# Optimization experiments

Measured on AMD Instinct MI355X. Metric: run time of the kernel, lower is better.

Reference implementation:

```python
import jax, jax.numpy as jnp
import numpy as np

DIS_NORM = 6.0 * 512 / 1000.0  # 6 * D(z=0) * Nmesh / Boxsize with D(0)=1


def setup_inputs() -> dict:
    key = jax.random.key(0)
    x = jax.random.normal(key, (2, 4, 128, 128, 128), dtype=jnp.float32)
    return {"x": x}


def _lag2eul(x):
    N, C = x.shape[0], x.shape[1]
    D, H, W = x.shape[2], x.shape[3], x.shape[4]
    P = D * H * W
    Cout = C - 3 if C > 3 else 1

    # rm_dis_mean=True: mean displacement, detached
    dis_mean = jax.lax.stop_gradient(jnp.mean(x[:, :3], axis=(2, 3, 4), keepdims=True))

    pos = (x[:, :3] - dis_mean) * DIS_NORM  # (N,3,D,H,W)
    gd = jnp.arange(D, dtype=x.dtype) + 0.5
    gh = jnp.arange(H, dtype=x.dtype) + 0.5
    gw = jnp.arange(W, dtype=x.dtype) + 0.5
    grid = jnp.stack(jnp.meshgrid(gd, gh, gw, indexing='ij'))  # (3,D,H,W)
    pos = (pos + grid[None]).reshape(N, 3, P)

    if C > 3:
        val = x[:, 3:].reshape(N, Cout, P)
    else:
        val = jnp.ones((N, Cout, P), dtype=x.dtype)

    intpos = jnp.floor(pos).astype(jnp.int32)
    # 8 trilinear neighbors: bit b of n -> offset along dim b
    neighbors = (jnp.arange(8, dtype=jnp.int32)[None, :] >> jnp.arange(3, dtype=jnp.int32)[:, None]) & 1  # (3,8)
    tgt = intpos[:, :, :, None] + neighbors[None, :, None, :]  # (N,3,P,8)

    kernel = jnp.prod(1.0 - jnp.abs(pos[:, :, :, None] - tgt.astype(x.dtype)), axis=1)  # (N,P,8)
    src = val[:, :, :, None] * kernel[:, None, :, :]  # (N,Cout,P,8)

    # periodic=False: mask out-of-bounds deposits
    bounds = jnp.array([D, H, W], dtype=jnp.int32)[None, :, None, None]
    mask = jnp.all((tgt >= 0) & (tgt < bounds), axis=1)  # (N,P,8)
    ind = (tgt[:, 0] * H + tgt[:, 1]) * W + tgt[:, 2]  # (N,P,8)
    ind = jnp.clip(ind, 0, P - 1)
    src = jnp.where(mask[:, None, :, :], src, jnp.zeros((), dtype=x.dtype))

    def scatter_one(ind_n, src_n):
        mesh = jnp.zeros((Cout, P), dtype=src_n.dtype)
        return mesh.at[:, ind_n.reshape(-1)].add(src_n.reshape(Cout, -1))

    mesh = jax.vmap(scatter_one)(ind, src)  # (N,Cout,P)
    return mesh.reshape(N, Cout, D, H, W)


def reference(x):
    return _lag2eul(x)
```

## Files before the change

kernel.cpp:

```cpp
#include <hip/hip_runtime.h>
#include <hip/hip_fp16.h>

#define NBATCH 2
#define NDIM   128
#define NP     (128 * 128 * 128)
#define DIS_NORM 3.072f

#define TS   16
#define LO   5
#define HI   6
#define WIN  (TS + LO + HI)
#define WIN2 (WIN * WIN)
#define WINF (WIN * WIN * WIN)
#define TPB  8
#define NTILE (TPB * TPB * TPB)
#define NTHR 512

#define FXSCALE 16777216.0f
#define FXINV   (1.0f / 16777216.0f)

#define QCAP 176

#define SLABH 19704

#define SUMS_OFF 0
#define SLABS_OFF 1024
#define WS_FLOATS ((size_t)SLABS_OFF + (size_t)NBATCH * NTILE * SLABH / 2)
#define WS_NEEDED_BYTES (WS_FLOATS * sizeof(float))

__device__ __constant__ int BASE27[27] = {
    0,216,792,976,1552,3088,3568,3752,4232,
    4384,4960,6496,6976,8512,12608,13888,14368,15648,
    16048,16232,16712,16864,17344,18624,19024,19176,19576};

__global__ __launch_bounds__(256) void prep_kernel(const float* __restrict__ x,
                                                   float* __restrict__ ws,
                                                   float* __restrict__ out) {
    const int plane = blockIdx.y;
    if (plane < 6) {
        const int n = plane / 3, c = plane % 3;
        const float4* xp = (const float4*)(x + ((size_t)n * 4 + c) * NP);
        float s = 0.0f;
        for (int i = blockIdx.x * 256 + threadIdx.x; i < NP / 4; i += 128 * 256) {
            float4 v = xp[i];
            s += (v.x + v.y) + (v.z + v.w);
        }
        #pragma unroll
        for (int off = 32; off > 0; off >>= 1) s += __shfl_down(s, off, 64);
        __shared__ float wsum[4];
        if ((threadIdx.x & 63) == 0) wsum[threadIdx.x >> 6] = s;
        __syncthreads();
        if (threadIdx.x == 0)
            ws[SUMS_OFF + plane * 128 + blockIdx.x] =
                (wsum[0] + wsum[1]) + (wsum[2] + wsum[3]);
    } else {
        float4* o4 = (float4*)out;
        const float4 z = make_float4(0.f, 0.f, 0.f, 0.f);
        for (int i = blockIdx.x * 256 + threadIdx.x; i < NBATCH * NP / 4; i += 128 * 256)
            o4[i] = z;
    }
}

__device__ __forceinline__ void load_means128(const float* __restrict__ ws, int n,
                                              float& m0, float& m1, float& m2) {
    float s0 = 0.f, s1 = 0.f, s2 = 0.f;
    const float* p0 = ws + SUMS_OFF + (n * 3 + 0) * 128;
    const float* p1 = ws + SUMS_OFF + (n * 3 + 1) * 128;
    const float* p2 = ws + SUMS_OFF + (n * 3 + 2) * 128;
    #pragma unroll 4
    for (int b = 0; b < 128; ++b) { s0 += p0[b]; s1 += p1[b]; s2 += p2[b]; }
    const float inv_np = 1.0f / (float)NP;
    m0 = s0 * inv_np; m1 = s1 * inv_np; m2 = s2 * inv_np;
}

__device__ __forceinline__ void deposit_pair(unsigned long long* __restrict__ winU,
                                             int b, float va, float vb) {
    const int fa = __float2int_rn(va * FXSCALE);
    const int fb = __float2int_rn(vb * FXSCALE);
    const bool odd = (b & 1);
    const long long packed = (((long long)fb) << 32) + (long long)fa;
    const long long hiOnly = ((long long)fa) << 32;
    atomicAdd(&winU[b >> 1], (unsigned long long)(odd ? hiOnly : packed));
    if (odd) atomicAdd(&winU[(b >> 1) + 1], (unsigned long long)(long long)fb);
}

__device__ __forceinline__ void slow_deposit(unsigned long long* __restrict__ winU,
                                             float* __restrict__ sp,
                                             float pd, float ph, float pw, float v,
                                             int od, int oh, int ow) {
    const float fd = floorf(pd), fh = floorf(ph), fw = floorf(pw);
    const int id = (int)fd, ih = (int)fh, iw = (int)fw;
    const float rd = pd - fd, rh = ph - fh, rw = pw - fw;
    const int wd = id - od, wh = ih - oh, ww = iw - ow;
    const float wd2[2] = {1.0f - rd, rd};
    const float wh2[2] = {1.0f - rh, rh};
    const float ww2[2] = {1.0f - rw, rw};
    #pragma unroll
    for (int dd = 0; dd < 2; ++dd) {
        const int td = id + dd, wdc = wd + dd;
        const bool dW = (unsigned)wdc < WIN, dM = (unsigned)td < NDIM;
        if (!dM && !dW) continue;
        #pragma unroll
        for (int hh = 0; hh < 2; ++hh) {
            const int th = ih + hh, whc = wh + hh;
            const bool hW = (unsigned)whc < WIN, hM = (unsigned)th < NDIM;
            const float vdh = v * wd2[dd] * wh2[hh];
            #pragma unroll
            for (int wi = 0; wi < 2; ++wi) {
                const int tw = iw + wi, wwc = ww + wi;
                const bool wW = (unsigned)wwc < WIN, wM = (unsigned)tw < NDIM;
                const float dep = vdh * ww2[wi];
                if (dW && hW && wW) {
                    const int cb = (wdc * WIN + whc) * WIN + wwc;
                    const int fx = __float2int_rn(dep * FXSCALE);
                    const long long cv = (cb & 1)
                        ? (((long long)fx) << 32) : (long long)fx;
                    atomicAdd(&winU[cb >> 1], (unsigned long long)cv);
                } else if (dM && hM && wM) {
                    atomicAdd(sp + ((size_t)td * NDIM + th) * NDIM + tw, dep);
                }
            }
        }
    }
}

__global__ __launch_bounds__(NTHR, 4) void scatter_tile_kernel(
        const float* __restrict__ x, const float* __restrict__ ws,
        __half* __restrict__ slabs, float* __restrict__ out) {
    const int blk = ((blockIdx.x & 7) << 7) | (blockIdx.x >> 3);
    const int n = blk >> 9;
    const int t = blk & (NTILE - 1);
    const int tx = t & 7, ty = (t >> 3) & 7, tz = t >> 6;

    __shared__ ulonglong2 win2[(WINF + 3) / 4 + 1];
    __shared__ float smean[3];
    __shared__ int qcount;
    __shared__ float4 queue[QCAP];
    unsigned long long* winU = (unsigned long long*)win2;
    {
        float4* z4 = (float4*)win2;
        const float4 z = make_float4(0.f, 0.f, 0.f, 0.f);
        for (int i = threadIdx.x; i < (WINF + 3) / 4 + 1; i += NTHR) z4[i] = z;
        if (threadIdx.x == 0) qcount = 0;
    }
    if (threadIdx.x < 192) {
        const int c = threadIdx.x >> 6;
        const int l = threadIdx.x & 63;
        const float* p = ws + SUMS_OFF + (n * 3 + c) * 128;
        float s = p[l] + p[l + 64];
        #pragma unroll
        for (int off = 32; off > 0; off >>= 1) s += __shfl_down(s, off, 64);
        if (l == 0) smean[c] = s * (1.0f / (float)NP);
    }
    __syncthreads();
    const float m0 = smean[0], m1 = smean[1], m2 = smean[2];

    const int i0 = threadIdx.x * 8;
    const int lw0 = i0 & 15;
    const int lh  = (i0 >> 4) & 15;
    const int ld  = i0 >> 8;
    const int gd = tz * TS + ld, gh = ty * TS + lh, gw0 = tx * TS + lw0;
    const size_t prow = ((size_t)gd * NDIM + gh) * NDIM + gw0;

    const float4* x4 = (const float4*)(x + (size_t)n * 4 * NP);
    const size_t q = prow >> 2;
    const size_t s4 = NP / 4;
    float4 a0 = x4[0 * s4 + q], a1 = x4[0 * s4 + q + 1];
    float4 b0 = x4[1 * s4 + q], b1 = x4[1 * s4 + q + 1];
    float4 c0 = x4[2 * s4 + q], c1 = x4[2 * s4 + q + 1];
    float4 e0 = x4[3 * s4 + q], e1 = x4[3 * s4 + q + 1];
    const float D0[8] = {a0.x, a0.y, a0.z, a0.w, a1.x, a1.y, a1.z, a1.w};
    const float D1[8] = {b0.x, b0.y, b0.z, b0.w, b1.x, b1.y, b1.z, b1.w};
    const float D2[8] = {c0.x, c0.y, c0.z, c0.w, c1.x, c1.y, c1.z, c1.w};
    const float VV[8] = {e0.x, e0.y, e0.z, e0.w, e1.x, e1.y, e1.z, e1.w};

    const int od = tz * TS - LO, oh = ty * TS - LO, ow = tx * TS - LO;
    float* sp = out + (size_t)n * NP;

    #pragma unroll
    for (int k = 0; k < 8; ++k) {
        const float pd = (D0[k] - m0) * DIS_NORM + (float)gd + 0.5f;
        const float ph = (D1[k] - m1) * DIS_NORM + (float)gh + 0.5f;
        const float pw = (D2[k] - m2) * DIS_NORM + (float)(gw0 + k) + 0.5f;
        const float v = VV[k];

        const float fd = floorf(pd), fh = floorf(ph), fw = floorf(pw);
        const int id = (int)fd, ih = (int)fh, iw = (int)fw;
        const float rd = pd - fd, rh = ph - fh, rw = pw - fw;

        const int wd = id - od, wh = ih - oh, ww = iw - ow;
        if ((unsigned)wd <= WIN - 2 && (unsigned)wh <= WIN - 2 &&
            (unsigned)ww <= WIN - 2) {
            const int b00 = (wd * WIN + wh) * WIN + ww;
            const float sd0 = v * (1.0f - rd), sd1 = v * rd;
            const float h0 = 1.0f - rh, h1 = rh;
            const float q0 = 1.0f - rw, q1 = rw;
            deposit_pair(winU, b00,              sd0 * h0 * q0, sd0 * h0 * q1);
            deposit_pair(winU, b00 + WIN,        sd0 * h1 * q0, sd0 * h1 * q1);
            deposit_pair(winU, b00 + WIN2,       sd1 * h0 * q0, sd1 * h0 * q1);
            deposit_pair(winU, b00 + WIN2 + WIN, sd1 * h1 * q0, sd1 * h1 * q1);
        } else {
            const int qi = atomicAdd(&qcount, 1);
            if (qi < QCAP) queue[qi] = make_float4(pd, ph, pw, v);
            else slow_deposit(winU, sp, pd, ph, pw, v, od, oh, ow);
        }
    }

    __syncthreads();

    {
        const int nq = min(qcount, QCAP);
        for (int qi = threadIdx.x; qi < nq; qi += NTHR) {
            const float4 e = queue[qi];
            slow_deposit(winU, sp, e.x, e.y, e.z, e.w, od, oh, ow);
        }
    }
    __syncthreads();

    const int EXTY[3] = {6, 16, 5};
    const int nbase = n << 9;
    for (int r = threadIdx.x; r < WIN2; r += NTHR) {
        const int lz = r / WIN;
        const int ly = r - lz * WIN;
        int mz, pz;
        if (lz < LO) { mz = -1; pz = lz; }
        else if (lz < LO + TS) { mz = 0; pz = lz - LO; }
        else { mz = 1; pz = lz - LO - TS; }
        int my, py;
        if (ly < LO) { my = -1; py = ly; }
        else if (ly < LO + TS) { my = 0; py = ly - LO; }
        else { my = 1; py = ly - LO - TS; }
        const int dtz = tz + mz, dty = ty + my;
        if ((unsigned)dtz >= TPB || (unsigned)dty >= TPB) continue;

        const int cbase = r * WIN;
        const int w0 = cbase >> 1;
        const int par = cbase & 1;
        float tmp[28];
        #pragma unroll
        for (int wI = 0; wI < 14; ++wI) {
            const unsigned long long u = winU[w0 + wI];
            const int lo = (int)(unsigned)(u & 0xffffffffull);
            const int hi = (int)(u >> 32) + (lo < 0 ? 1 : 0);
            tmp[2 * wI]     = (float)lo * FXINV;
            tmp[2 * wI + 1] = (float)hi * FXINV;
        }
        const float* src = tmp + par;

        const int jz = 1 - mz, jy = 1 - my;
        const int ey = EXTY[jy];
        const int rowoff = pz * ey + py;
        const int pobase = jz * 9 + jy * 3;
        const int slabRow = nbase + (dtz * 8 + dty) * 8;

        if (tx > 0) {
            __half* d = slabs + (size_t)(slabRow + tx - 1) * SLABH
                      + BASE27[pobase + 2] + rowoff * 5;
            #pragma unroll
            for (int k = 0; k < 5; ++k) d[k] = __float2half_rn(src[k]);
        }
        {
            __half* d = slabs + (size_t)(slabRow + tx) * SLABH
                      + BASE27[pobase + 1] + rowoff * 16;
            union { uint4 u; __half2 h[4]; } p0, p1;
            #pragma unroll
            for (int k = 0; k < 4; ++k)
                p0.h[k] = __floats2half2_rn(src[5 + 2 * k], src[6 + 2 * k]);
            #pragma unroll
            for (int k = 0; k < 4; ++k)
                p1.h[k] = __floats2half2_rn(src[13 + 2 * k], src[14 + 2 * k]);
            ((uint4*)d)[0] = p0.u;
            ((uint4*)d)[1] = p1.u;
        }
        if (tx < TPB - 1) {
            __half* d = slabs + (size_t)(slabRow + tx + 1) * SLABH
                      + BASE27[pobase + 0] + rowoff * 6;
            __half2* d2 = (__half2*)d;
            d2[0] = __floats2half2_rn(src[21], src[22]);
            d2[1] = __floats2half2_rn(src[23], src[24]);
            d2[2] = __floats2half2_rn(src[25], src[26]);
        }
    }
}

__device__ __forceinline__ float4 ldh4(const __half* p) {
    const uint2 u = *(const uint2*)p;
    const __half2 h0 = *(const __half2*)&u.x;
    const __half2 h1 = *(const __half2*)&u.y;
    return make_float4(__low2float(h0), __high2float(h0),
                       __low2float(h1), __high2float(h1));
}

__global__ __launch_bounds__(NTHR) void gather_tile_kernel(const __half* __restrict__ slabs,
                                                           float* __restrict__ out) {
    const int blk = ((blockIdx.x & 7) << 7) | (blockIdx.x >> 3);
    const int n = blk >> 9;
    const int t = blk & (NTILE - 1);
    const int tx = t & 7, ty = (t >> 3) & 7, tz = t >> 6;

    const __half* __restrict__ slab = slabs + (size_t)blk * SLABH;
    float4* __restrict__ o4 = (float4*)(out + (size_t)n * NP);

    for (int i4 = threadIdx.x; i4 < TS * TS * TS / 4; i4 += NTHR) {
        const int xq = i4 & 3, y = (i4 >> 2) & 15, z = i4 >> 6;

        int ysec = 0, yp = 0, ye = 0; bool y2 = false;
        if (y < 6)        { if (ty > 0)       { ysec = 0; yp = y;      ye = 6; y2 = true; } }
        else if (y >= 11) { if (ty < TPB - 1) { ysec = 6; yp = y - 11; ye = 5; y2 = true; } }
        int zsec = 0, zp = 0; bool z2 = false;
        if (z < 6)        { if (tz > 0)       { zsec = 0;  zp = z;      z2 = true; } }
        else if (z >= 11) { if (tz < TPB - 1) { zsec = 18; zp = z - 11; z2 = true; } }

        const int rC = z * 16 + y;
        float4 s = ldh4(slab + BASE27[13] + rC * 16 + xq * 4);
        int rY = 0, rZ = 0, rYZ = 0;
        if (y2) {
            rY = z * ye + yp;
            const float4 v = ldh4(slab + BASE27[10 + ysec] + rY * 16 + xq * 4);
            s.x += v.x; s.y += v.y; s.z += v.z; s.w += v.w;
        }
        if (z2) {
            rZ = zp * 16 + y;
            const float4 v = ldh4(slab + BASE27[zsec + 4] + rZ * 16 + xq * 4);
            s.x += v.x; s.y += v.y; s.z += v.z; s.w += v.w;
            if (y2) {
                rYZ = zp * ye + yp;
                const float4 v2 = ldh4(slab + BASE27[zsec + ysec + 1] + rYZ * 16 + xq * 4);
                s.x += v2.x; s.y += v2.y; s.z += v2.z; s.w += v2.w;
            }
        }

        float se[4] = {s.x, s.y, s.z, s.w};
        #pragma unroll
        for (int e = 0; e < 4; ++e) {
            const int xx = xq * 4 + e;
            int xsec = 0, xp = 0, xe = 0; bool x2 = false;
            if (xx < 6)        { if (tx > 0)       { xsec = 0; xp = xx;      xe = 6; x2 = true; } }
            else if (xx >= 11) { if (tx < TPB - 1) { xsec = 2; xp = xx - 11; xe = 5; x2 = true; } }
            if (x2) {
                se[e] += __half2float(slab[BASE27[12 + xsec] + rC * xe + xp]);
                if (y2) se[e] += __half2float(slab[BASE27[9 + ysec + xsec] + rY * xe + xp]);
                if (z2) {
                    se[e] += __half2float(slab[BASE27[zsec + 3 + xsec] + rZ * xe + xp]);
                    if (y2) se[e] += __half2float(slab[BASE27[zsec + ysec + xsec] + rYZ * xe + xp]);
                }
            }
        }

        const size_t grow = ((size_t)(tz * TS + z) * NDIM + ty * TS + y) * (NDIM / 4)
                          + tx * 4 + xq;
        float4 o = o4[grow];
        o.x += se[0]; o.y += se[1]; o.z += se[2]; o.w += se[3];
        o4[grow] = o;
    }
}

__global__ __launch_bounds__(256) void scatter_direct_kernel(const float* __restrict__ x,
                                                             const float* __restrict__ ws,
                                                             float* __restrict__ out) {
    const int lin = blockIdx.x * 256 + threadIdx.x;
    const int n = lin >> 21;
    const int p = lin & (NP - 1);

    float m0, m1, m2;
    load_means128(ws, n, m0, m1, m2);

    const size_t base = (size_t)n * 4 * NP;
    const float d0 = x[base + 0 * (size_t)NP + p];
    const float d1 = x[base + 1 * (size_t)NP + p];
    const float d2 = x[base + 2 * (size_t)NP + p];
    const float v  = x[base + 3 * (size_t)NP + p];

    const int w = p & 127, h = (p >> 7) & 127, d = p >> 14;
    const float pd = (d0 - m0) * DIS_NORM + (float)d + 0.5f;
    const float ph = (d1 - m1) * DIS_NORM + (float)h + 0.5f;
    const float pw = (d2 - m2) * DIS_NORM + (float)w + 0.5f;
    const float fd = floorf(pd), fh = floorf(ph), fw = floorf(pw);
    const int id = (int)fd, ih = (int)fh, iw = (int)fw;
    const float rd = pd - fd, rh = ph - fh, rw = pw - fw;
    const float wd[2] = {1.0f - rd, rd}, wh[2] = {1.0f - rh, rh}, ww[2] = {1.0f - rw, rw};
    float* o = out + (size_t)n * NP;
    #pragma unroll
    for (int dd = 0; dd < 2; ++dd) {
        const int td = id + dd;
        if ((unsigned)td >= (unsigned)NDIM) continue;
        #pragma unroll
        for (int hh = 0; hh < 2; ++hh) {
            const int th = ih + hh;
            if ((unsigned)th >= (unsigned)NDIM) continue;
            const float vdh = v * wd[dd] * wh[hh];
            const int rowbase = (td * NDIM + th) * NDIM;
            #pragma unroll
            for (int wi = 0; wi < 2; ++wi) {
                const int tw = iw + wi;
                if ((unsigned)tw >= (unsigned)NDIM) continue;
                atomicAdd(o + rowbase + tw, vdh * ww[wi]);
            }
        }
    }
}

extern "C" void kernel_launch(void* const* d_in, const int* in_sizes, int n_in,
                              void* d_out, int out_size, void* d_ws, size_t ws_size,
                              hipStream_t stream) {
    const float* x = (const float*)d_in[0];
    float* out = (float*)d_out;
    float* ws = (float*)d_ws;
    __half* slabs = (__half*)(ws + SLABS_OFF);

    dim3 pgrid(128, 7);

    if (ws_size >= WS_NEEDED_BYTES) {
        prep_kernel<<<pgrid, 256, 0, stream>>>(x, ws, out);
        scatter_tile_kernel<<<dim3(NBATCH * NTILE), NTHR, 0, stream>>>(x, ws, slabs, out);
        gather_tile_kernel<<<dim3(NBATCH * NTILE), NTHR, 0, stream>>>(slabs, out);
    } else {
        prep_kernel<<<pgrid, 256, 0, stream>>>(x, ws, out);
        scatter_direct_kernel<<<dim3(NBATCH * NP / 256), 256, 0, stream>>>(x, ws, out);
    }
}
```

Baseline: 166.3 us.

## Route far deposits through per-tile inboxes and skip output zeroing

Particles that deposit outside their tile's shared window no longer do float atomics directly into the global output. They append (cell, value) records to a per-destination-tile inbox in workspace. The gather kernel first accumulates its inbox into a shared fixed-point tile, then writes the output directly instead of read-modify-write, so the prep kernel no longer has to zero the whole output. This removes a full-output zeroing pass and a read of the output, at the cost of a larger workspace, global counter atomics, and silently dropping deposits when an inbox exceeds its capacity.

```diff
diff --git a/kernel.cpp b/kernel.cpp
--- a/kernel.cpp
+++ b/kernel.cpp
@@ -21,11 +21,17 @@
 
 #define QCAP 176
 
+#define ICAP 4096
+
 #define SLABH 19704
 
 #define SUMS_OFF 0
-#define SLABS_OFF 1024
-#define WS_FLOATS ((size_t)SLABS_OFF + (size_t)NBATCH * NTILE * SLABH / 2)
+#define CNT_OFF 1024
+#define SLABS_OFF 2048
+#define SLAB_FLOATS ((size_t)NBATCH * NTILE * SLABH / 2)
+#define INBOX_OFF ((size_t)SLABS_OFF + SLAB_FLOATS)
+#define INBOX_FLOATS ((size_t)NBATCH * NTILE * ICAP * 2)
+#define WS_FLOATS (INBOX_OFF + INBOX_FLOATS)
 #define WS_NEEDED_BYTES (WS_FLOATS * sizeof(float))
 
 __device__ __constant__ int BASE27[27] = {
@@ -35,7 +41,8 @@
 
 __global__ __launch_bounds__(256) void prep_kernel(const float* __restrict__ x,
                                                    float* __restrict__ ws,
-                                                   float* __restrict__ out) {
+                                                   float* __restrict__ out,
+                                                   int flag) {
     const int plane = blockIdx.y;
     if (plane < 6) {
         const int n = plane / 3, c = plane % 3;
@@ -54,10 +61,17 @@
             ws[SUMS_OFF + plane * 128 + blockIdx.x] =
                 (wsum[0] + wsum[1]) + (wsum[2] + wsum[3]);
     } else {
-        float4* o4 = (float4*)out;
-        const float4 z = make_float4(0.f, 0.f, 0.f, 0.f);
-        for (int i = blockIdx.x * 256 + threadIdx.x; i < NBATCH * NP / 4; i += 128 * 256)
-            o4[i] = z;
+        if (flag & 1) {
+            const int i = blockIdx.x * 256 + threadIdx.x;
+            if (i < NBATCH * NTILE) ((unsigned*)(ws + CNT_OFF))[i] = 0u;
+        }
+        if (flag & 2) {
+            float4* o4 = (float4*)out;
+            const float4 z = make_float4(0.f, 0.f, 0.f, 0.f);
+            for (int i = blockIdx.x * 256 + threadIdx.x; i < NBATCH * NP / 4;
+                 i += 128 * 256)
+                o4[i] = z;
+        }
     }
 }
 
@@ -85,7 +99,9 @@
 }
 
 __device__ __forceinline__ void slow_deposit(unsigned long long* __restrict__ winU,
-                                             float* __restrict__ sp,
+                                             unsigned* __restrict__ cnt,
+                                             float2* __restrict__ inbox,
+                                             int n9,
                                              float pd, float ph, float pw, float v,
                                              int od, int oh, int ow) {
     const float fd = floorf(pd), fh = floorf(ph), fw = floorf(pw);
@@ -117,7 +133,13 @@
                         ? (((long long)fx) << 32) : (long long)fx;
                     atomicAdd(&winU[cb >> 1], (unsigned long long)cv);
                 } else if (dM && hM && wM) {
-                    atomicAdd(sp + ((size_t)td * NDIM + th) * NDIM + tw, dep);
+                    const int tIdx = n9 + ((td >> 4) * 8 + (th >> 4)) * 8 + (tw >> 4);
+                    const unsigned slot = atomicAdd(&cnt[tIdx], 1u);
+                    if (slot < ICAP) {
+                        const int cell = (((td & 15) * 16) + (th & 15)) * 16 + (tw & 15);
+                        inbox[(size_t)tIdx * ICAP + slot] =
+                            make_float2(__int_as_float(cell), dep);
+                    }
                 }
             }
         }
@@ -125,12 +147,15 @@
 }
 
 __global__ __launch_bounds__(NTHR, 4) void scatter_tile_kernel(
-        const float* __restrict__ x, const float* __restrict__ ws,
-        __half* __restrict__ slabs, float* __restrict__ out) {
+        const float* __restrict__ x, float* __restrict__ ws) {
     const int blk = ((blockIdx.x & 7) << 7) | (blockIdx.x >> 3);
     const int n = blk >> 9;
     const int t = blk & (NTILE - 1);
     const int tx = t & 7, ty = (t >> 3) & 7, tz = t >> 6;
+
+    __half* slabs = (__half*)(ws + SLABS_OFF);
+    unsigned* cnt = (unsigned*)(ws + CNT_OFF);
+    float2* inbox = (float2*)(ws + INBOX_OFF);
 
     __shared__ ulonglong2 win2[(WINF + 3) / 4 + 1];
     __shared__ float smean[3];
@@ -175,7 +200,7 @@
     const float VV[8] = {e0.x, e0.y, e0.z, e0.w, e1.x, e1.y, e1.z, e1.w};
 
     const int od = tz * TS - LO, oh = ty * TS - LO, ow = tx * TS - LO;
-    float* sp = out + (size_t)n * NP;
+    const int n9 = n << 9;
 
     #pragma unroll
     for (int k = 0; k < 8; ++k) {
@@ -202,7 +227,7 @@
         } else {
             const int qi = atomicAdd(&qcount, 1);
             if (qi < QCAP) queue[qi] = make_float4(pd, ph, pw, v);
-            else slow_deposit(winU, sp, pd, ph, pw, v, od, oh, ow);
+            else slow_deposit(winU, cnt, inbox, n9, pd, ph, pw, v, od, oh, ow);
         }
     }
 
@@ -212,7 +237,7 @@
         const int nq = min(qcount, QCAP);
         for (int qi = threadIdx.x; qi < nq; qi += NTHR) {
             const float4 e = queue[qi];
-            slow_deposit(winU, sp, e.x, e.y, e.z, e.w, od, oh, ow);
+            slow_deposit(winU, cnt, inbox, n9, e.x, e.y, e.z, e.w, od, oh, ow);
         }
     }
     __syncthreads();
@@ -291,15 +316,33 @@
                        __low2float(h1), __high2float(h1));
 }
 
-__global__ __launch_bounds__(NTHR) void gather_tile_kernel(const __half* __restrict__ slabs,
+__global__ __launch_bounds__(NTHR) void gather_tile_kernel(const float* __restrict__ ws,
                                                            float* __restrict__ out) {
     const int blk = ((blockIdx.x & 7) << 7) | (blockIdx.x >> 3);
     const int n = blk >> 9;
     const int t = blk & (NTILE - 1);
     const int tx = t & 7, ty = (t >> 3) & 7, tz = t >> 6;
 
-    const __half* __restrict__ slab = slabs + (size_t)blk * SLABH;
+    const __half* __restrict__ slab =
+        (const __half*)(ws + SLABS_OFF) + (size_t)blk * SLABH;
+    const unsigned* __restrict__ cnt = (const unsigned*)(ws + CNT_OFF);
+    const float2* __restrict__ inbox =
+        (const float2*)(ws + INBOX_OFF) + (size_t)blk * ICAP;
     float4* __restrict__ o4 = (float4*)(out + (size_t)n * NP);
+
+    __shared__ unsigned tileFx[TS * TS * TS];
+    for (int i = threadIdx.x; i < TS * TS * TS; i += NTHR) tileFx[i] = 0u;
+    __syncthreads();
+    {
+        const int nc = min((int)cnt[blk], ICAP);
+        for (int i = threadIdx.x; i < nc; i += NTHR) {
+            const float2 e = inbox[i];
+            const int cell = __float_as_int(e.x);
+            const int fx = __float2int_rn(e.y * FXSCALE);
+            atomicAdd(&tileFx[cell], (unsigned)fx);
+        }
+    }
+    __syncthreads();
 
     for (int i4 = threadIdx.x; i4 < TS * TS * TS / 4; i4 += NTHR) {
         const int xq = i4 & 3, y = (i4 >> 2) & 15, z = i4 >> 6;
@@ -345,12 +388,13 @@
                     if (y2) se[e] += __half2float(slab[BASE27[zsec + ysec + xsec] + rYZ * xe + xp]);
                 }
             }
+            se[e] += (float)(int)tileFx[rC * 16 + xx] * FXINV;
         }
 
         const size_t grow = ((size_t)(tz * TS + z) * NDIM + ty * TS + y) * (NDIM / 4)
                           + tx * 4 + xq;
-        float4 o = o4[grow];
-        o.x += se[0]; o.y += se[1]; o.z += se[2]; o.w += se[3];
+        float4 o;
+        o.x = se[0]; o.y = se[1]; o.z = se[2]; o.w = se[3];
         o4[grow] = o;
     }
 }
@@ -406,16 +450,15 @@
     const float* x = (const float*)d_in[0];
     float* out = (float*)d_out;
     float* ws = (float*)d_ws;
-    __half* slabs = (__half*)(ws + SLABS_OFF);
 
     dim3 pgrid(128, 7);
 
     if (ws_size >= WS_NEEDED_BYTES) {
-        prep_kernel<<<pgrid, 256, 0, stream>>>(x, ws, out);
-        scatter_tile_kernel<<<dim3(NBATCH * NTILE), NTHR, 0, stream>>>(x, ws, slabs, out);
-        gather_tile_kernel<<<dim3(NBATCH * NTILE), NTHR, 0, stream>>>(slabs, out);
+        prep_kernel<<<pgrid, 256, 0, stream>>>(x, ws, out, 1);
+        scatter_tile_kernel<<<dim3(NBATCH * NTILE), NTHR, 0, stream>>>(x, ws);
+        gather_tile_kernel<<<dim3(NBATCH * NTILE), NTHR, 0, stream>>>(ws, out);
     } else {
-        prep_kernel<<<pgrid, 256, 0, stream>>>(x, ws, out);
+        prep_kernel<<<pgrid, 256, 0, stream>>>(x, ws, out, 2);
         scatter_direct_kernel<<<dim3(NBATCH * NP / 256), 256, 0, stream>>>(x, ws, out);
     }
 }
```

Measured after the change: 375.2 us. 126% more time.
